# Kernel optimization log

Hardware: AMD Instinct MI355X
Metric: run time of the kernel (lower is better)

## Reference

```python
import jax, jax.numpy as jnp
import numpy as np

N = 50000
E = 800000
D_IN = 256
HID = 64
HEADS = 4
OUT = 86
EPS_BN = 1e-5
NEG_SLOPE = 0.2


def setup_inputs() -> dict:
    key = jax.random.key(0)
    ks = jax.random.split(key, 16)
    HC = HEADS * HID
    inp = {
        "x": jax.random.normal(ks[0], (N, D_IN), jnp.float32),
        "edge_index": jax.random.randint(ks[1], (2, E), 0, N, jnp.int64),
        # GATConv 1: in=D_IN, out per head=HID, concat=True
        "W1": jax.random.normal(ks[2], (D_IN, HC), jnp.float32) * (1.0 / np.sqrt(D_IN)),
        "att_src1": jax.random.normal(ks[3], (HEADS, HID), jnp.float32) * 0.1,
        "att_dst1": jax.random.normal(ks[4], (HEADS, HID), jnp.float32) * 0.1,
        "b1": jnp.zeros((HC,), jnp.float32),
        # GATConv 2: in=HC, out per head=HID, concat=False (mean over heads)
        "W2": jax.random.normal(ks[5], (HC, HC), jnp.float32) * (1.0 / np.sqrt(HC)),
        "att_src2": jax.random.normal(ks[6], (HEADS, HID), jnp.float32) * 0.1,
        "att_dst2": jax.random.normal(ks[7], (HEADS, HID), jnp.float32) * 0.1,
        "b2": jnp.zeros((HID,), jnp.float32),
        # BatchNorms
        "g1": jnp.ones((HC,), jnp.float32),
        "be1": jnp.zeros((HC,), jnp.float32),
        "g2": jnp.ones((HID,), jnp.float32),
        "be2": jnp.zeros((HID,), jnp.float32),
        # PReLU (single shared weight, torch default init 0.25)
        "prelu_w": jnp.asarray(0.25, jnp.float32),
        # final Linear
        "fcW": jax.random.normal(ks[8], (HID, OUT), jnp.float32) * (1.0 / np.sqrt(HID)),
        "fcb": jnp.zeros((OUT,), jnp.float32),
    }
    return inp


def _gat_conv(x, src, dst, W, att_src, att_dst, bias, concat):
    # PyG GATConv forward (dropout inactive in eval mode).
    n = x.shape[0]
    H, C = att_src.shape
    h = (x @ W).reshape(n, H, C)                      # [N,H,C]
    a_s = jnp.sum(h * att_src[None], axis=-1)         # [N,H]
    a_d = jnp.sum(h * att_dst[None], axis=-1)         # [N,H]
    logits = jax.nn.leaky_relu(a_s[src] + a_d[dst], NEG_SLOPE)  # [E,H]
    # segment softmax over edges grouped by destination node
    m = jax.ops.segment_max(logits, dst, num_segments=n)        # [N,H]
    e = jnp.exp(logits - m[dst])
    s = jax.ops.segment_sum(e, dst, num_segments=n)             # [N,H]
    alpha = e / (s[dst] + 1e-16)                                # [E,H]
    msg = h[src] * alpha[:, :, None]                            # [E,H,C]
    out = jax.ops.segment_sum(msg, dst, num_segments=n)         # [N,H,C]
    if concat:
        return out.reshape(n, H * C) + bias
    return out.mean(axis=1) + bias


def _batch_norm(x, gamma, beta):
    mu = x.mean(axis=0)
    var = x.var(axis=0)
    return gamma * (x - mu) * jax.lax.rsqrt(var + EPS_BN) + beta


def reference(x, edge_index, W1, att_src1, att_dst1, b1, W2, att_src2, att_dst2, b2,
              g1, be1, g2, be2, prelu_w, fcW, fcb):
    n = x.shape[0]
    # GATConv default add_self_loops=True
    loops = jnp.arange(n, dtype=edge_index.dtype)
    src = jnp.concatenate([edge_index[0], loops])
    dst = jnp.concatenate([edge_index[1], loops])

    h = _gat_conv(x, src, dst, W1, att_src1, att_dst1, b1, concat=True)
    h = _batch_norm(h, g1, be1)
    h = jnp.where(h >= 0, h, prelu_w * h)             # PReLU
    # dropout: identity (eval)
    h = _gat_conv(h, src, dst, W2, att_src2, att_dst2, b2, concat=False)
    h = _batch_norm(h, g2, be2)
    h = jax.nn.elu(h)
    return h @ fcW + fcb
```

## Files before the change

kernel.cpp:

```cpp
#include <hip/hip_runtime.h>
#include <math.h>

#define LEAKY 0.2f

typedef __attribute__((ext_vector_type(8))) short short8;
typedef __attribute__((ext_vector_type(4))) float f32x4;

__device__ __forceinline__ float leaky02(float z) { return z >= 0.f ? z : LEAKY * z; }
__device__ __forceinline__ unsigned short f2bf(float f) {
  unsigned u = __float_as_uint(f);
  unsigned r = u + 0x7fffu + ((u >> 16) & 1u);
  return (unsigned short)(r >> 16);
}
__device__ __forceinline__ float bflo(unsigned u) { return __uint_as_float(u << 16); }
__device__ __forceinline__ float bfhi(unsigned u) { return __uint_as_float(u & 0xffff0000u); }

__global__ void count_kernel(const int* __restrict__ ei, int* __restrict__ cnt, int E, int N) {
  int e = blockIdx.x * 256 + threadIdx.x;
  int EP = E + N;
  if (e >= EP) return;
  int d = (e < E) ? ei[E + e] : (e - E);
  atomicAdd(&cnt[d], 1);
}

__global__ __launch_bounds__(256) void scan1_kernel(const int* __restrict__ cnt,
                                                    int* __restrict__ bsums, int n) {
  int i = blockIdx.x * 256 + threadIdx.x;
  int v = (i < n) ? cnt[i] : 0;
  int lane = threadIdx.x & 63, wv = threadIdx.x >> 6;
#pragma unroll
  for (int off = 32; off; off >>= 1) v += __shfl_xor(v, off);
  __shared__ int w[4];
  if (lane == 0) w[wv] = v;
  __syncthreads();
  if (threadIdx.x == 0) bsums[blockIdx.x] = w[0] + w[1] + w[2] + w[3];
}

__global__ __launch_bounds__(256) void scan2_kernel(int* __restrict__ bsums, int nb) {
  int tid = threadIdx.x;
  int lane = tid & 63, wv = tid >> 6;
  int v = (tid < nb) ? bsums[tid] : 0;
  int x = v;
#pragma unroll
  for (int off = 1; off < 64; off <<= 1) {
    int t = __shfl_up(x, off);
    if (lane >= off) x += t;
  }
  __shared__ int ws[4];
  if (lane == 63) ws[wv] = x;
  __syncthreads();
  int woff = 0;
#pragma unroll
  for (int w = 0; w < 4; ++w) if (w < wv) woff += ws[w];
  if (tid < nb) bsums[tid] = x + woff - v;
}

__global__ __launch_bounds__(256) void scan3_kernel(const int* __restrict__ cnt,
                                                    const int* __restrict__ boff,
                                                    int* __restrict__ rowptr,
                                                    int* __restrict__ cursor, int n) {
  int i = blockIdx.x * 256 + threadIdx.x;
  int tid = threadIdx.x, lane = tid & 63, wv = tid >> 6;
  int v = (i < n) ? cnt[i] : 0;
  int x = v;
#pragma unroll
  for (int off = 1; off < 64; off <<= 1) {
    int t = __shfl_up(x, off);
    if (lane >= off) x += t;
  }
  __shared__ int ws[4];
  if (lane == 63) ws[wv] = x;
  __syncthreads();
  int woff = 0;
#pragma unroll
  for (int w = 0; w < 4; ++w) if (w < wv) woff += ws[w];
  int incl = x + woff;
  int base = boff[blockIdx.x];
  if (i < n) {
    rowptr[i + 1] = base + incl;
    cursor[i] = base + incl - v;
  }
  if (i == 0) rowptr[0] = 0;
}

__global__ void fill_kernel(const int* __restrict__ ei, int* __restrict__ cursor,
                            int* __restrict__ srcs, int E, int N) {
  int e = blockIdx.x * 256 + threadIdx.x;
  int EP = E + N;
  if (e >= EP) return;
  int s, d;
  if (e < E) { s = ei[e]; d = ei[E + e]; } else { s = e - E; d = s; }
  int slot = atomicAdd(&cursor[d], 1);
  srcs[slot] = s;
}

__global__ void convw_kernel(const float* __restrict__ W1, const float* __restrict__ W2,
                             unsigned short* __restrict__ Wt1, unsigned short* __restrict__ Wt2) {
  int idx = blockIdx.x * 256 + threadIdx.x;
  const float* W;
  unsigned short* Wt;
  if (idx < 65536) { W = W1; Wt = Wt1; } else { W = W2; Wt = Wt2; idx -= 65536; }
  int c = idx >> 8, k = idx & 255;
  Wt[c * 256 + k] = f2bf(W[k * 256 + c]);
}

template <bool BF16A>
__global__ __launch_bounds__(512) void gemm_kernel(const void* __restrict__ Av,
                                                   const unsigned short* __restrict__ Wt,
                                                   unsigned short* __restrict__ Hout, int M,
                                                   const float* __restrict__ bnsc,
                                                   const float* __restrict__ bnsh,
                                                   const float* __restrict__ pwp,
                                                   const float* __restrict__ att_s,
                                                   const float* __restrict__ att_d,
                                                   float* __restrict__ as_o,
                                                   float* __restrict__ ad_o) {
  __shared__ unsigned short As[128][40];
  __shared__ unsigned short Bs[256][40];
  int tid = threadIdx.x;
  int bm = blockIdx.x * 128;
  int l = tid & 63, wv = tid >> 6;
  int wm = wv >> 2, wn = wv & 3;
  int lr = l & 15, lk = l >> 4;
  f32x4 acc[4][4] = {};
  bool hasbn = (bnsc != nullptr);
  float pws = pwp ? pwp[0] : 0.f;

  for (int k0 = 0; k0 < 256; k0 += 32) {
    {
      int row = tid >> 2, kq = (tid & 3) * 8;
      int gr = bm + row;
      if (BF16A) {
        uint4 u = make_uint4(0, 0, 0, 0);
        if (gr < M) u = *(const uint4*)((const unsigned short*)Av + (size_t)gr * 256 + k0 + kq);
        if (hasbn) {
          float4 sc0 = *(const float4*)&bnsc[k0 + kq];
          float4 sh0 = *(const float4*)&bnsh[k0 + kq];
          float4 sc1 = *(const float4*)&bnsc[k0 + kq + 4];
          float4 sh1 = *(const float4*)&bnsh[k0 + kq + 4];
          float v0 = fmaf(bflo(u.x), sc0.x, sh0.x);
          float v1 = fmaf(bfhi(u.x), sc0.y, sh0.y);
          float v2 = fmaf(bflo(u.y), sc0.z, sh0.z);
          float v3 = fmaf(bfhi(u.y), sc0.w, sh0.w);
          float v4 = fmaf(bflo(u.z), sc1.x, sh1.x);
          float v5 = fmaf(bfhi(u.z), sc1.y, sh1.y);
          float v6 = fmaf(bflo(u.w), sc1.z, sh1.z);
          float v7 = fmaf(bfhi(u.w), sc1.w, sh1.w);
          v0 = v0 >= 0.f ? v0 : v0 * pws; v1 = v1 >= 0.f ? v1 : v1 * pws;
          v2 = v2 >= 0.f ? v2 : v2 * pws; v3 = v3 >= 0.f ? v3 : v3 * pws;
          v4 = v4 >= 0.f ? v4 : v4 * pws; v5 = v5 >= 0.f ? v5 : v5 * pws;
          v6 = v6 >= 0.f ? v6 : v6 * pws; v7 = v7 >= 0.f ? v7 : v7 * pws;
          ushort4 o0, o1;
          o0.x = f2bf(v0); o0.y = f2bf(v1); o0.z = f2bf(v2); o0.w = f2bf(v3);
          o1.x = f2bf(v4); o1.y = f2bf(v5); o1.z = f2bf(v6); o1.w = f2bf(v7);
          *(ushort4*)&As[row][kq] = o0;
          *(ushort4*)&As[row][kq + 4] = o1;
        } else {
          *(uint4*)&As[row][kq] = u;
        }
      } else {
        float4 a0 = make_float4(0.f, 0.f, 0.f, 0.f), a1 = a0;
        if (gr < M) {
          a0 = *(const float4*)((const float*)Av + (size_t)gr * 256 + k0 + kq);
          a1 = *(const float4*)((const float*)Av + (size_t)gr * 256 + k0 + kq + 4);
        }
        ushort4 o0, o1;
        o0.x = f2bf(a0.x); o0.y = f2bf(a0.y); o0.z = f2bf(a0.z); o0.w = f2bf(a0.w);
        o1.x = f2bf(a1.x); o1.y = f2bf(a1.y); o1.z = f2bf(a1.z); o1.w = f2bf(a1.w);
        *(ushort4*)&As[row][kq] = o0;
        *(ushort4*)&As[row][kq + 4] = o1;
      }
    }
#pragma unroll
    for (int it = 0; it < 2; ++it) {
      int i = tid + it * 512;
      int c = i >> 2, kq = (i & 3) * 8;
      *(uint4*)&Bs[c][kq] = *(const uint4*)&Wt[(size_t)c * 256 + k0 + kq];
    }
    __syncthreads();
    short8 af[4], bfr[4];
#pragma unroll
    for (int mt = 0; mt < 4; ++mt) af[mt] = *(const short8*)&As[wm * 64 + mt * 16 + lr][lk * 8];
#pragma unroll
    for (int nt = 0; nt < 4; ++nt) bfr[nt] = *(const short8*)&Bs[wn * 64 + nt * 16 + lr][lk * 8];
#pragma unroll
    for (int mt = 0; mt < 4; ++mt)
#pragma unroll
      for (int nt = 0; nt < 4; ++nt)
        acc[mt][nt] = __builtin_amdgcn_mfma_f32_16x16x32_bf16(af[mt], bfr[nt], acc[mt][nt], 0, 0, 0);
    __syncthreads();
  }
  float asv[4], adv[4];
#pragma unroll
  for (int nt = 0; nt < 4; ++nt) {
    int gc = wn * 64 + nt * 16 + lr;
    asv[nt] = att_s[gc];
    adv[nt] = att_d[gc];
  }
#pragma unroll
  for (int mt = 0; mt < 4; ++mt) {
#pragma unroll
    for (int r = 0; r < 4; ++r) {
      int gr = bm + wm * 64 + mt * 16 + lk * 4 + r;
      float ps = acc[mt][0][r] * asv[0] + acc[mt][1][r] * asv[1] +
                 acc[mt][2][r] * asv[2] + acc[mt][3][r] * asv[3];
      float pd = acc[mt][0][r] * adv[0] + acc[mt][1][r] * adv[1] +
                 acc[mt][2][r] * adv[2] + acc[mt][3][r] * adv[3];
#pragma unroll
      for (int off = 1; off < 16; off <<= 1) {
        ps += __shfl_xor(ps, off);
        pd += __shfl_xor(pd, off);
      }
      if (lr == 0 && gr < M) {
        as_o[gr * 4 + wn] = ps;
        ad_o[gr * 4 + wn] = pd;
      }
      if (gr < M) {
#pragma unroll
        for (int nt = 0; nt < 4; ++nt)
          Hout[(size_t)gr * 256 + wn * 64 + nt * 16 + lr] = f2bf(acc[mt][nt][r]);
      }
    }
  }
}

__global__ __launch_bounds__(256) void agg_kernel(const unsigned short* __restrict__ h,
                                                  const float* __restrict__ as_,
                                                  const float* __restrict__ ad_,
                                                  const int* __restrict__ rowptr,
                                                  const int* __restrict__ srcs,
                                                  const float* __restrict__ bias,
                                                  unsigned short* __restrict__ out_bf,
                                                  float* __restrict__ out_f,
                                                  int N, int concat) {
  int l = threadIdx.x & 63;
  int n = blockIdx.x * 4 + (threadIdx.x >> 6);
  if (n >= N) return;
  int e0 = rowptr[n], e1 = rowptr[n + 1];
  int deg = e1 - e0;
  int hh = l >> 4, le = l & 15;
  float adh = ad_[n * 4 + hh];

  if (deg <= 64) {
    int sidx[4];
    float lg[4];
#pragma unroll
    for (int t = 0; t < 4; ++t) {
      int j = e0 + le + 16 * t;
      if (j < e1) {
        int s = srcs[j];
        sidx[t] = s;
        lg[t] = leaky02(as_[s * 4 + hh] + adh);
      } else {
        sidx[t] = 0;
        lg[t] = -1e30f;
      }
    }
    float mx = fmaxf(fmaxf(lg[0], lg[1]), fmaxf(lg[2], lg[3]));
#pragma unroll
    for (int off = 1; off < 16; off <<= 1) mx = fmaxf(mx, __shfl_xor(mx, off));
    float ex[4];
    float sm = 0.f;
#pragma unroll
    for (int t = 0; t < 4; ++t) {
      ex[t] = (lg[t] > -1e29f) ? __expf(lg[t] - mx) : 0.f;
      sm += ex[t];
    }
#pragma unroll
    for (int off = 1; off < 16; off <<= 1) sm += __shfl_xor(sm, off);
    float inv = 1.f / (sm + 1e-16f);

    int p = l >> 5, m = l & 31;
    int hb = m >> 3;
    float invb = __shfl(inv, hb << 4);
    float a[8] = {0.f, 0.f, 0.f, 0.f, 0.f, 0.f, 0.f, 0.f};
#pragma unroll
    for (int t = 0; t < 4; ++t) {
      int base = e0 + 16 * t;
      if (base >= e1) break;
      int cntc = min(16, e1 - base);
      int npr = (cntc + 1) >> 1;
      for (int pr = 0; pr < npr; ++pr) {
        int q = 2 * pr + p;
        int s = __shfl(sidx[t], q);
        float al = __shfl(ex[t], q + (hb << 4)) * invb;
        uint4 hv = *(const uint4*)&h[(size_t)s * 256 + m * 8];
        a[0] = fmaf(bflo(hv.x), al, a[0]);
        a[1] = fmaf(bfhi(hv.x), al, a[1]);
        a[2] = fmaf(bflo(hv.y), al, a[2]);
        a[3] = fmaf(bfhi(hv.y), al, a[3]);
        a[4] = fmaf(bflo(hv.z), al, a[4]);
        a[5] = fmaf(bfhi(hv.z), al, a[5]);
        a[6] = fmaf(bflo(hv.w), al, a[6]);
        a[7] = fmaf(bfhi(hv.w), al, a[7]);
      }
    }
#pragma unroll
    for (int i = 0; i < 8; ++i) a[i] += __shfl_xor(a[i], 32);
    if (concat) {
      if (l < 32) {
        float4 b0 = *(const float4*)&bias[m * 8];
        float4 b1 = *(const float4*)&bias[m * 8 + 4];
        ushort4 o0, o1;
        o0.x = f2bf(a[0] + b0.x); o0.y = f2bf(a[1] + b0.y);
        o0.z = f2bf(a[2] + b0.z); o0.w = f2bf(a[3] + b0.w);
        o1.x = f2bf(a[4] + b1.x); o1.y = f2bf(a[5] + b1.y);
        o1.z = f2bf(a[6] + b1.z); o1.w = f2bf(a[7] + b1.w);
        *(ushort4*)&out_bf[(size_t)n * 256 + m * 8] = o0;
        *(ushort4*)&out_bf[(size_t)n * 256 + m * 8 + 4] = o1;
      }
    } else {
#pragma unroll
      for (int i = 0; i < 8; ++i) {
        a[i] += __shfl_xor(a[i], 8);
        a[i] += __shfl_xor(a[i], 16);
      }
      if (l < 8) {
        float4 b0 = *(const float4*)&bias[m * 8];
        float4 b1 = *(const float4*)&bias[m * 8 + 4];
        float4 o0 = make_float4(0.25f * a[0] + b0.x, 0.25f * a[1] + b0.y,
                                0.25f * a[2] + b0.z, 0.25f * a[3] + b0.w);
        float4 o1 = make_float4(0.25f * a[4] + b1.x, 0.25f * a[5] + b1.y,
                                0.25f * a[6] + b1.z, 0.25f * a[7] + b1.w);
        *(float4*)&out_f[(size_t)n * 64 + m * 8] = o0;
        *(float4*)&out_f[(size_t)n * 64 + m * 8 + 4] = o1;
      }
    }
  } else {
    float ad4[4] = {ad_[n * 4], ad_[n * 4 + 1], ad_[n * 4 + 2], ad_[n * 4 + 3]};
    float mx[4] = {-1e30f, -1e30f, -1e30f, -1e30f};
    for (int j = e0 + l; j < e1; j += 64) {
      int s = srcs[j];
      float4 av = *(const float4*)&as_[s * 4];
      mx[0] = fmaxf(mx[0], leaky02(av.x + ad4[0]));
      mx[1] = fmaxf(mx[1], leaky02(av.y + ad4[1]));
      mx[2] = fmaxf(mx[2], leaky02(av.z + ad4[2]));
      mx[3] = fmaxf(mx[3], leaky02(av.w + ad4[3]));
    }
#pragma unroll
    for (int off = 32; off; off >>= 1) {
      mx[0] = fmaxf(mx[0], __shfl_xor(mx[0], off));
      mx[1] = fmaxf(mx[1], __shfl_xor(mx[1], off));
      mx[2] = fmaxf(mx[2], __shfl_xor(mx[2], off));
      mx[3] = fmaxf(mx[3], __shfl_xor(mx[3], off));
    }
    float sm[4] = {0.f, 0.f, 0.f, 0.f};
    for (int j = e0 + l; j < e1; j += 64) {
      int s = srcs[j];
      float4 av = *(const float4*)&as_[s * 4];
      sm[0] += __expf(leaky02(av.x + ad4[0]) - mx[0]);
      sm[1] += __expf(leaky02(av.y + ad4[1]) - mx[1]);
      sm[2] += __expf(leaky02(av.z + ad4[2]) - mx[2]);
      sm[3] += __expf(leaky02(av.w + ad4[3]) - mx[3]);
    }
#pragma unroll
    for (int off = 32; off; off >>= 1) {
      sm[0] += __shfl_xor(sm[0], off);
      sm[1] += __shfl_xor(sm[1], off);
      sm[2] += __shfl_xor(sm[2], off);
      sm[3] += __shfl_xor(sm[3], off);
    }
    float mh = hh == 0 ? mx[0] : hh == 1 ? mx[1] : hh == 2 ? mx[2] : mx[3];
    float sh = hh == 0 ? sm[0] : hh == 1 ? sm[1] : hh == 2 ? sm[2] : sm[3];
    float inv = 1.f / (sh + 1e-16f);
    float a0 = 0.f, a1 = 0.f, a2 = 0.f, a3 = 0.f;
    for (int j = e0; j < e1; ++j) {
      int s = srcs[j];
      float al = __expf(leaky02(as_[s * 4 + hh] + adh) - mh) * inv;
      uint2 hv = *(const uint2*)&h[(size_t)s * 256 + l * 4];
      a0 = fmaf(bflo(hv.x), al, a0); a1 = fmaf(bfhi(hv.x), al, a1);
      a2 = fmaf(bflo(hv.y), al, a2); a3 = fmaf(bfhi(hv.y), al, a3);
    }
    if (concat) {
      float4 b4 = *(const float4*)&bias[l * 4];
      ushort4 o;
      o.x = f2bf(a0 + b4.x); o.y = f2bf(a1 + b4.y);
      o.z = f2bf(a2 + b4.z); o.w = f2bf(a3 + b4.w);
      *(ushort4*)&out_bf[(size_t)n * 256 + l * 4] = o;
    } else {
      a0 += __shfl_xor(a0, 16); a0 += __shfl_xor(a0, 32);
      a1 += __shfl_xor(a1, 16); a1 += __shfl_xor(a1, 32);
      a2 += __shfl_xor(a2, 16); a2 += __shfl_xor(a2, 32);
      a3 += __shfl_xor(a3, 16); a3 += __shfl_xor(a3, 32);
      if (l < 16) {
        float4 b4 = *(const float4*)&bias[l * 4];
        float4 o = make_float4(0.25f * a0 + b4.x, 0.25f * a1 + b4.y,
                               0.25f * a2 + b4.z, 0.25f * a3 + b4.w);
        *(float4*)&out_f[(size_t)n * 64 + l * 4] = o;
      }
    }
  }
}

__global__ __launch_bounds__(256) void bnstats_bf16_kernel(const unsigned short* __restrict__ x,
                                                           float* __restrict__ sum,
                                                           float* __restrict__ ss, int N) {
  int tid = threadIdx.x;
  int c = (tid & 127) * 2;
  int r = blockIdx.x * 2 + (tid >> 7);
  int stride = gridDim.x * 2;
  float a0 = 0.f, b0 = 0.f, a1 = 0.f, b1 = 0.f;
  for (; r < N; r += stride) {
    unsigned u = *(const unsigned*)&x[(size_t)r * 256 + c];
    float v0 = bflo(u), v1 = bfhi(u);
    a0 += v0; b0 += v0 * v0;
    a1 += v1; b1 += v1 * v1;
  }
  atomicAdd(&sum[c], a0); atomicAdd(&ss[c], b0);
  atomicAdd(&sum[c + 1], a1); atomicAdd(&ss[c + 1], b1);
}

__global__ __launch_bounds__(256) void bnstats_kernel(const float* __restrict__ x,
                                                      float* __restrict__ sum, float* __restrict__ ss,
                                                      int N, int C) {
  int tid = threadIdx.x;
  int f = tid % C;
  int rpb = 256 / C;
  int r = blockIdx.x * rpb + tid / C;
  int stride = gridDim.x * rpb;
  float a = 0.f, b = 0.f;
  for (; r < N; r += stride) {
    float v = x[(size_t)r * C + f];
    a += v;
    b += v * v;
  }
  atomicAdd(&sum[f], a);
  atomicAdd(&ss[f], b);
}

__global__ void bnfinalize_kernel(const float* __restrict__ sum, const float* __restrict__ ss,
                                  const float* __restrict__ gamma, const float* __restrict__ beta,
                                  float* __restrict__ scale, float* __restrict__ shift, int N, int C) {
  int f = threadIdx.x;
  if (f >= C) return;
  float mu = sum[f] / (float)N;
  float var = ss[f] / (float)N - mu * mu;
  float sc = gamma[f] * rsqrtf(var + 1e-5f);
  scale[f] = sc;
  shift[f] = beta[f] - mu * sc;
}

__global__ __launch_bounds__(256) void fc_kernel(const float* __restrict__ x,
                                                 const float* __restrict__ sc, const float* __restrict__ sh,
                                                 const float* __restrict__ W, const float* __restrict__ b,
                                                 float* __restrict__ out, int N) {
  __shared__ float ws[64 * 86];
  __shared__ float xs[32 * 64];
  int tid = threadIdx.x;
  for (int i = tid; i < 64 * 86; i += 256) ws[i] = W[i];
  int n0 = blockIdx.x * 32;
  for (int i = tid; i < 32 * 64; i += 256) {
    int n = n0 + (i >> 6), c = i & 63;
    float v = (n < N) ? x[(size_t)n * 64 + c] : 0.f;
    v = fmaf(v, sc[c], sh[c]);
    xs[i] = v > 0.f ? v : expm1f(v);
  }
  __syncthreads();
  for (int idx = tid; idx < 32 * 86; idx += 256) {
    int nl = idx / 86, o = idx % 86;
    int n = n0 + nl;
    if (n >= N) continue;
    float acc = b[o];
    const float* xr = &xs[nl * 64];
#pragma unroll 8
    for (int k = 0; k < 64; ++k) acc = fmaf(xr[k], ws[k * 86 + o], acc);
    out[(size_t)n * 86 + o] = acc;
  }
}

extern "C" void kernel_launch(void* const* d_in, const int* in_sizes, int n_in,
                              void* d_out, int out_size, void* d_ws, size_t ws_size,
                              hipStream_t stream) {
  const float* x    = (const float*)d_in[0];
  const int*   ei   = (const int*)d_in[1];
  const float* W1   = (const float*)d_in[2];
  const float* asw1 = (const float*)d_in[3];
  const float* adw1 = (const float*)d_in[4];
  const float* b1   = (const float*)d_in[5];
  const float* W2   = (const float*)d_in[6];
  const float* asw2 = (const float*)d_in[7];
  const float* adw2 = (const float*)d_in[8];
  const float* b2   = (const float*)d_in[9];
  const float* g1   = (const float*)d_in[10];
  const float* be1  = (const float*)d_in[11];
  const float* g2   = (const float*)d_in[12];
  const float* be2  = (const float*)d_in[13];
  const float* pw   = (const float*)d_in[14];
  const float* fcW  = (const float*)d_in[15];
  const float* fcb  = (const float*)d_in[16];

  const int N = in_sizes[0] / 256;
  const int E = in_sizes[1] / 2;
  const int EP = E + N;

  char* ws = (char*)d_ws;
  size_t off = 0;
  auto alloc = [&](size_t bytes) {
    char* p = ws + off;
    off += (bytes + 255) & ~(size_t)255;
    return p;
  };
  unsigned short* h    = (unsigned short*)alloc((size_t)N * 256 * 2);
  unsigned short* outb = (unsigned short*)alloc((size_t)N * 256 * 2);
  float* xm   = (float*)alloc((size_t)N * 64 * 4);
  float* as1  = (float*)alloc((size_t)N * 4 * 4);
  float* ad1  = (float*)alloc((size_t)N * 4 * 4);
  float* as2  = (float*)alloc((size_t)N * 4 * 4);
  float* ad2  = (float*)alloc((size_t)N * 4 * 4);
  int* rowptr = (int*)alloc((size_t)(N + 1) * 4);
  int* cnt    = (int*)alloc((size_t)N * 4);
  int* cursor = (int*)alloc((size_t)N * 4);
  int* srcs   = (int*)alloc((size_t)EP * 4);
  int* bsums  = (int*)alloc(1024 * 4);
  unsigned short* Wt1 = (unsigned short*)alloc(65536 * 2);
  unsigned short* Wt2 = (unsigned short*)alloc(65536 * 2);
  float* bstat = (float*)alloc(512 * 4);
  float* bsum = bstat, *bss = bstat + 256;
  float* bsc  = (float*)alloc(256 * 4);
  float* bsh  = (float*)alloc(256 * 4);
  float* bsc2 = (float*)alloc(64 * 4);
  float* bsh2 = (float*)alloc(64 * 4);

  int egrid = (EP + 255) / 256;
  int ngrid4 = (N + 3) / 4;
  int nb = (N + 255) / 256;
  int ggrid = (N + 127) / 128;

  hipMemsetAsync(cnt, 0, (size_t)N * 4, stream);
  count_kernel<<<egrid, 256, 0, stream>>>(ei, cnt, E, N);
  convw_kernel<<<512, 256, 0, stream>>>(W1, W2, Wt1, Wt2);
  scan1_kernel<<<nb, 256, 0, stream>>>(cnt, bsums, N);
  scan2_kernel<<<1, 256, 0, stream>>>(bsums, nb);
  scan3_kernel<<<nb, 256, 0, stream>>>(cnt, bsums, rowptr, cursor, N);
  fill_kernel<<<egrid, 256, 0, stream>>>(ei, cursor, srcs, E, N);

  gemm_kernel<false><<<ggrid, 512, 0, stream>>>(x, Wt1, h, N, nullptr, nullptr, nullptr,
                                                asw1, adw1, as1, ad1);
  agg_kernel<<<ngrid4, 256, 0, stream>>>(h, as1, ad1, rowptr, srcs, b1, outb, nullptr, N, 1);

  hipMemsetAsync(bstat, 0, 512 * 4, stream);
  bnstats_bf16_kernel<<<512, 256, 0, stream>>>(outb, bsum, bss, N);
  bnfinalize_kernel<<<1, 256, 0, stream>>>(bsum, bss, g1, be1, bsc, bsh, N, 256);

  gemm_kernel<true><<<ggrid, 512, 0, stream>>>(outb, Wt2, h, N, bsc, bsh, pw,
                                               asw2, adw2, as2, ad2);
  agg_kernel<<<ngrid4, 256, 0, stream>>>(h, as2, ad2, rowptr, srcs, b2, nullptr, xm, N, 0);

  hipMemsetAsync(bstat, 0, 128 * 4, stream);
  bnstats_kernel<<<512, 256, 0, stream>>>(xm, bstat, bstat + 64, N, 64);
  bnfinalize_kernel<<<1, 64, 0, stream>>>(bstat, bstat + 64, g2, be2, bsc2, bsh2, N, 64);

  fc_kernel<<<(N + 31) / 32, 256, 0, stream>>>(xm, bsc2, bsh2, fcW, fcb, (float*)d_out, N);
}
```

Measured before the change: 565.8 us.

## Build CSR via two-level bucket sort with shared-memory atomics

Replaces the per-node global-atomic count, three-pass scan and atomic fill with a bucketed counting sort. Edges are first bucketed by destination/256 using shared-memory histograms, then each bucket is sorted locally into CSR order inside one block. This cuts contended global atomics and random scattered writes, at the cost of an extra pass over the edges and a packed intermediate pairs buffer. The packing assumes source indices fit in 24 bits and at most 256 buckets (N up to 65536). Unlike the atomic fill, within-node edge order is now deterministic per block, but it still depends on atomic ordering.

```diff
diff --git a/kernel.cpp b/kernel.cpp
--- a/kernel.cpp
+++ b/kernel.cpp
@@ -2,6 +2,7 @@
 #include <math.h>
 
 #define LEAKY 0.2f
+#define NBMAX 256
 
 typedef __attribute__((ext_vector_type(8))) short short8;
 typedef __attribute__((ext_vector_type(4))) float f32x4;
@@ -15,31 +16,31 @@
 __device__ __forceinline__ float bflo(unsigned u) { return __uint_as_float(u << 16); }
 __device__ __forceinline__ float bfhi(unsigned u) { return __uint_as_float(u & 0xffff0000u); }
 
-__global__ void count_kernel(const int* __restrict__ ei, int* __restrict__ cnt, int E, int N) {
-  int e = blockIdx.x * 256 + threadIdx.x;
+
+__global__ __launch_bounds__(256) void bktcount_kernel(const int* __restrict__ ei,
+                                                       int* __restrict__ bucketCnt,
+                                                       int E, int N, int NB) {
+  __shared__ int bc[NBMAX];
+  for (int i = threadIdx.x; i < NB; i += 256) bc[i] = 0;
+  __syncthreads();
   int EP = E + N;
-  if (e >= EP) return;
-  int d = (e < E) ? ei[E + e] : (e - E);
-  atomicAdd(&cnt[d], 1);
-}
-
-__global__ __launch_bounds__(256) void scan1_kernel(const int* __restrict__ cnt,
-                                                    int* __restrict__ bsums, int n) {
-  int i = blockIdx.x * 256 + threadIdx.x;
-  int v = (i < n) ? cnt[i] : 0;
-  int lane = threadIdx.x & 63, wv = threadIdx.x >> 6;
-#pragma unroll
-  for (int off = 32; off; off >>= 1) v += __shfl_xor(v, off);
-  __shared__ int w[4];
-  if (lane == 0) w[wv] = v;
-  __syncthreads();
-  if (threadIdx.x == 0) bsums[blockIdx.x] = w[0] + w[1] + w[2] + w[3];
-}
-
-__global__ __launch_bounds__(256) void scan2_kernel(int* __restrict__ bsums, int nb) {
+  int chunk = (EP + gridDim.x - 1) / gridDim.x;
+  int lo = blockIdx.x * chunk, hi = min(EP, lo + chunk);
+  for (int e = lo + threadIdx.x; e < hi; e += 256) {
+    int d = (e < E) ? ei[E + e] : (e - E);
+    atomicAdd(&bc[d >> 8], 1);
+  }
+  __syncthreads();
+  for (int i = threadIdx.x; i < NB; i += 256)
+    if (bc[i]) atomicAdd(&bucketCnt[i], bc[i]);
+}
+
+__global__ __launch_bounds__(256) void bktscan_kernel(const int* __restrict__ bucketCnt,
+                                                      int* __restrict__ bucketOff,
+                                                      int* __restrict__ bucketCur, int NB) {
   int tid = threadIdx.x;
   int lane = tid & 63, wv = tid >> 6;
-  int v = (tid < nb) ? bsums[tid] : 0;
+  int v = (tid < NB) ? bucketCnt[tid] : 0;
   int x = v;
 #pragma unroll
   for (int off = 1; off < 64; off <<= 1) {
@@ -52,16 +53,61 @@
   int woff = 0;
 #pragma unroll
   for (int w = 0; w < 4; ++w) if (w < wv) woff += ws[w];
-  if (tid < nb) bsums[tid] = x + woff - v;
-}
-
-__global__ __launch_bounds__(256) void scan3_kernel(const int* __restrict__ cnt,
-                                                    const int* __restrict__ boff,
-                                                    int* __restrict__ rowptr,
-                                                    int* __restrict__ cursor, int n) {
-  int i = blockIdx.x * 256 + threadIdx.x;
-  int tid = threadIdx.x, lane = tid & 63, wv = tid >> 6;
-  int v = (i < n) ? cnt[i] : 0;
+  int incl = x + woff;
+  if (tid < NB) {
+    bucketOff[tid] = incl - v;
+    bucketCur[tid] = incl - v;
+  }
+  if (tid == NB - 1) bucketOff[NB] = incl;
+}
+
+__global__ __launch_bounds__(256) void bktscatter_kernel(const int* __restrict__ ei,
+                                                         int* __restrict__ bucketCur,
+                                                         unsigned* __restrict__ pairs,
+                                                         int E, int N, int NB) {
+  __shared__ int bc[NBMAX];
+  __shared__ int bbase[NBMAX];
+  for (int i = threadIdx.x; i < NB; i += 256) bc[i] = 0;
+  __syncthreads();
+  int EP = E + N;
+  int chunk = (EP + gridDim.x - 1) / gridDim.x;
+  int lo = blockIdx.x * chunk, hi = min(EP, lo + chunk);
+  for (int e = lo + threadIdx.x; e < hi; e += 256) {
+    int d = (e < E) ? ei[E + e] : (e - E);
+    atomicAdd(&bc[d >> 8], 1);
+  }
+  __syncthreads();
+  for (int i = threadIdx.x; i < NB; i += 256) {
+    int c = bc[i];
+    bbase[i] = c ? atomicAdd(&bucketCur[i], c) : 0;
+    bc[i] = 0;
+  }
+  __syncthreads();
+  for (int e = lo + threadIdx.x; e < hi; e += 256) {
+    int s, d;
+    if (e < E) { s = ei[e]; d = ei[E + e]; } else { s = e - E; d = s; }
+    int b = d >> 8;
+    int slot = bbase[b] + atomicAdd(&bc[b], 1);
+    pairs[slot] = ((unsigned)s << 8) | (unsigned)(d & 255);
+  }
+}
+
+__global__ __launch_bounds__(256) void bktcsr_kernel(const unsigned* __restrict__ pairs,
+                                                     const int* __restrict__ bucketOff,
+                                                     int* __restrict__ rowptr,
+                                                     int* __restrict__ srcs, int N, int NB) {
+  int b = blockIdx.x;
+  int tid = threadIdx.x;
+  __shared__ int cnt[256], loff[256], cur[256];
+  cnt[tid] = 0;
+  cur[tid] = 0;
+  __syncthreads();
+  int p0 = bucketOff[b], p1 = bucketOff[b + 1];
+  for (int j = p0 + tid; j < p1; j += 256)
+    atomicAdd(&cnt[pairs[j] & 255], 1);
+  __syncthreads();
+  int v = cnt[tid];
+  int lane = tid & 63, wv = tid >> 6;
   int x = v;
 #pragma unroll
   for (int off = 1; off < 64; off <<= 1) {
@@ -74,24 +120,18 @@
   int woff = 0;
 #pragma unroll
   for (int w = 0; w < 4; ++w) if (w < wv) woff += ws[w];
-  int incl = x + woff;
-  int base = boff[blockIdx.x];
-  if (i < n) {
-    rowptr[i + 1] = base + incl;
-    cursor[i] = base + incl - v;
-  }
-  if (i == 0) rowptr[0] = 0;
-}
-
-__global__ void fill_kernel(const int* __restrict__ ei, int* __restrict__ cursor,
-                            int* __restrict__ srcs, int E, int N) {
-  int e = blockIdx.x * 256 + threadIdx.x;
-  int EP = E + N;
-  if (e >= EP) return;
-  int s, d;
-  if (e < E) { s = ei[e]; d = ei[E + e]; } else { s = e - E; d = s; }
-  int slot = atomicAdd(&cursor[d], 1);
-  srcs[slot] = s;
+  int excl = x + woff - v;
+  loff[tid] = excl;
+  int node = (b << 8) + tid;
+  if (node < N) rowptr[node] = p0 + excl;
+  if (b == NB - 1 && tid == 255) rowptr[N] = p1;
+  __syncthreads();
+  for (int j = p0 + tid; j < p1; j += 256) {
+    unsigned pr = pairs[j];
+    int ln = pr & 255;
+    int slot = p0 + loff[ln] + atomicAdd(&cur[ln], 1);
+    srcs[slot] = pr >> 8;
+  }
 }
 
 __global__ void convw_kernel(const float* __restrict__ W1, const float* __restrict__ W2,
@@ -492,6 +532,7 @@
   const int N = in_sizes[0] / 256;
   const int E = in_sizes[1] / 2;
   const int EP = E + N;
+  const int NB = (N + 255) / 256;
 
   char* ws = (char*)d_ws;
   size_t off = 0;
@@ -508,10 +549,11 @@
   float* as2  = (float*)alloc((size_t)N * 4 * 4);
   float* ad2  = (float*)alloc((size_t)N * 4 * 4);
   int* rowptr = (int*)alloc((size_t)(N + 1) * 4);
-  int* cnt    = (int*)alloc((size_t)N * 4);
-  int* cursor = (int*)alloc((size_t)N * 4);
   int* srcs   = (int*)alloc((size_t)EP * 4);
-  int* bsums  = (int*)alloc(1024 * 4);
+  unsigned* pairs = (unsigned*)alloc((size_t)EP * 4);
+  int* bucketCnt = (int*)alloc((NBMAX + 1) * 4);
+  int* bucketOff = (int*)alloc((NBMAX + 1) * 4);
+  int* bucketCur = (int*)alloc((NBMAX + 1) * 4);
   unsigned short* Wt1 = (unsigned short*)alloc(65536 * 2);
   unsigned short* Wt2 = (unsigned short*)alloc(65536 * 2);
   float* bstat = (float*)alloc(512 * 4);
@@ -521,18 +563,15 @@
   float* bsc2 = (float*)alloc(64 * 4);
   float* bsh2 = (float*)alloc(64 * 4);
 
-  int egrid = (EP + 255) / 256;
   int ngrid4 = (N + 3) / 4;
-  int nb = (N + 255) / 256;
   int ggrid = (N + 127) / 128;
 
-  hipMemsetAsync(cnt, 0, (size_t)N * 4, stream);
-  count_kernel<<<egrid, 256, 0, stream>>>(ei, cnt, E, N);
+  hipMemsetAsync(bucketCnt, 0, (NBMAX + 1) * 4, stream);
+  bktcount_kernel<<<256, 256, 0, stream>>>(ei, bucketCnt, E, N, NB);
   convw_kernel<<<512, 256, 0, stream>>>(W1, W2, Wt1, Wt2);
-  scan1_kernel<<<nb, 256, 0, stream>>>(cnt, bsums, N);
-  scan2_kernel<<<1, 256, 0, stream>>>(bsums, nb);
-  scan3_kernel<<<nb, 256, 0, stream>>>(cnt, bsums, rowptr, cursor, N);
-  fill_kernel<<<egrid, 256, 0, stream>>>(ei, cursor, srcs, E, N);
+  bktscan_kernel<<<1, 256, 0, stream>>>(bucketCnt, bucketOff, bucketCur, NB);
+  bktscatter_kernel<<<256, 256, 0, stream>>>(ei, bucketCur, pairs, E, N, NB);
+  bktcsr_kernel<<<NB, 256, 0, stream>>>(pairs, bucketOff, rowptr, srcs, N, NB);
 
   gemm_kernel<false><<<ggrid, 512, 0, stream>>>(x, Wt1, h, N, nullptr, nullptr, nullptr,
                                                 asw1, adw1, as1, ad1);
```

After: 512.0 us. 9.5% less time.
